# Kernel tuning notes

Measured on AMD Instinct MI355X. Metric: run time of the kernel, lower is better.

The kernel has to match this reference:

```python
import jax, jax.numpy as jnp
import numpy as np

N, G, H = 500_000, 25_000, 256


def setup_inputs() -> dict:
    key = jax.random.key(0)
    ks = jax.random.split(key, 8)
    node = jax.random.normal(ks[0], (N, H), dtype=jnp.float32)
    super_node = jax.random.normal(ks[1], (G, H), dtype=jnp.float32)
    segment_ids = jnp.sort(jax.random.randint(ks[2], (N,), 0, G, dtype=jnp.int32))
    s = 0.05
    return {
        "node": node,
        "super_node": super_node,
        "segment_ids": segment_ids,
        "w_align": jax.random.normal(ks[3], (2 * H, 1), jnp.float32) * s,
        "b_align": jnp.zeros((1,), jnp.float32),
        "w_attend": jax.random.normal(ks[4], (H, H), jnp.float32) * s,
        "b_attend": jnp.zeros((H,), jnp.float32),
        "w_ih": jax.random.normal(ks[5], (H, 3 * H), jnp.float32) * s,
        "w_hh": jax.random.normal(ks[6], (H, 3 * H), jnp.float32) * s,
        "b_ih": jnp.zeros((3 * H,), jnp.float32),
        "b_hh": jnp.zeros((3 * H,), jnp.float32),
    }


def reference(node, super_node, segment_ids, w_align, b_align, w_attend,
              b_attend, w_ih, w_hh, b_ih, b_hh):
    g = super_node.shape[0]
    h = node.shape[1]
    # super_node = F.leaky_relu(super_node)
    s = jax.nn.leaky_relu(super_node)  # slope 0.01 (torch default)
    # cal_alignment(cat([node, broadcast_nodes(super)])) == node@Wn + (s@Ws)[seg]
    wn, ws = w_align[:h], w_align[h:]
    score = jax.nn.leaky_relu(node @ wn + (s @ ws)[segment_ids] + b_align)  # [N,1]
    # softmax_nodes: segment-wise stable softmax
    m = jax.ops.segment_max(score, segment_ids, num_segments=g)
    w = jnp.exp(score - m[segment_ids])
    denom = jax.ops.segment_sum(w, segment_ids, num_segments=g)
    attn = w / denom[segment_ids]  # [N,1]
    # attend (dropout=0, eval)
    hidden = node @ w_attend + b_attend  # [N,H]
    # sum_nodes weighted by attention, then ELU
    ctx = jax.nn.elu(jax.ops.segment_sum(attn * hidden, segment_ids, num_segments=g))  # [G,H]
    # GRUCell(ctx, s) per torch semantics
    gi = ctx @ w_ih + b_ih
    gh = s @ w_hh + b_hh
    ir, iz, inn = jnp.split(gi, 3, axis=-1)
    hr, hz, hn = jnp.split(gh, 3, axis=-1)
    r = jax.nn.sigmoid(ir + hr)
    z = jax.nn.sigmoid(iz + hz)
    n = jnp.tanh(inn + r * hn)
    new_h = (1.0 - z) * n + z * s
    return jax.nn.relu(new_h), attn
```

## Files before the change

### kernel.cpp

```cpp
#include <hip/hip_runtime.h>
#include <math.h>

#define N_NODES 500000
#define G_SEG   25000
#define H_DIM   256
#define SPB     4

typedef __attribute__((ext_vector_type(4))) float f32x4;
typedef __attribute__((ext_vector_type(8))) short bf16x8;

__device__ __forceinline__ float leaky(float x){ return x > 0.f ? x : 0.01f * x; }

__device__ __forceinline__ ushort f2bf(float f){
  unsigned u = __float_as_uint(f);
  u += 0x7FFFu + ((u >> 16) & 1u);
  return (ushort)(u >> 16);
}

__global__ __launch_bounds__(256) void k_starts(
    const int* __restrict__ seg, int* __restrict__ starts)
{
  int i = blockIdx.x * 256 + threadIdx.x;
  if (i >= N_NODES) return;
  int s = seg[i];
  int prev = (i == 0) ? -1 : seg[i - 1];
  for (int g = prev + 1; g <= s; g++) starts[g] = i;
  if (i == N_NODES - 1)
    for (int g = s + 1; g <= G_SEG; g++) starts[g] = N_NODES;
}

__global__ __launch_bounds__(256) void k0_prep_w(
    const float* __restrict__ w_att, ushort* __restrict__ Bp)
{
  int kk = blockIdx.x, n = threadIdx.x;
  Bp[(((kk >> 3) << 8) + n) * 8 + (kk & 7)] = f2bf(w_att[kk * H_DIM + n]);
}

__global__ __launch_bounds__(256) void k0b_prep_w6(
    const float* __restrict__ w_ih, const float* __restrict__ w_hh,
    ushort* __restrict__ Bp6)
{
  int kk = blockIdx.x;
  int c  = threadIdx.x;
  #pragma unroll
  for (int gate = 0; gate < 4; gate++) {
    float v;
    if (gate == 0)      v = (kk < 256) ? w_ih[kk * 768 + c]        : w_hh[(kk - 256) * 768 + c];
    else if (gate == 1) v = (kk < 256) ? w_ih[kk * 768 + 256 + c]  : w_hh[(kk - 256) * 768 + 256 + c];
    else if (gate == 2) v = (kk < 256) ? w_ih[kk * 768 + 512 + c]  : 0.f;
    else                v = (kk < 256) ? 0.f                       : w_hh[(kk - 256) * 768 + 512 + c];
    int n = (gate << 8) + c;
    Bp6[(((kk >> 3) << 10) + n) * 8 + (kk & 7)] = f2bf(v);
  }
}

__global__ __launch_bounds__(256) void k1_prep_super(
    const float* __restrict__ sn, const float* __restrict__ w_align,
    float* __restrict__ s_buf, float* __restrict__ sws)
{
  int g = blockIdx.x, t = threadIdx.x;
  float v = sn[g * H_DIM + t];
  float sv = leaky(v);
  s_buf[g * H_DIM + t] = sv;
  float p = sv * w_align[H_DIM + t];
  #pragma unroll
  for (int d = 1; d < 64; d <<= 1) p += __shfl_xor(p, d);
  __shared__ float red[4];
  int wid = t >> 6, lane = t & 63;
  if (lane == 0) red[wid] = p;
  __syncthreads();
  if (t == 0) sws[g] = red[0] + red[1] + red[2] + red[3];
}

__global__ __launch_bounds__(256) void kF_score_softmax_agg(
    const float* __restrict__ node, const int* __restrict__ starts,
    const float* __restrict__ w_align, const float* __restrict__ b_align,
    const float* __restrict__ sws, float* __restrict__ score,
    float* __restrict__ attn_out, float* __restrict__ agg,
    float* __restrict__ bscale)
{
  __shared__ float cpart[4][H_DIM];
  __shared__ float wm[4], wsum[4];
  __shared__ int st_s[SPB + 1];

  const int tid = threadIdx.x;
  const int g0 = blockIdx.x * SPB;
  if (tid <= SPB) st_s[tid] = starts[g0 + tid];
  __syncthreads();

  const int wv = tid >> 6, lane = tid & 63;
  const float4 wvec = ((const float4*)w_align)[lane];
  const float b0 = b_align[0];

  for (int j = 0; j < SPB; j++) {
    const int g = g0 + j;
    const int st = st_s[j], en = st_s[j + 1];
    const float swsg = sws[g];

    float m = -3.4e38f, sum = 0.f;
    f32x4 pacc = {0.f, 0.f, 0.f, 0.f};

    for (int r = st + wv; r < en; r += 4) {
      f32x4 a = ((const f32x4*)node)[(size_t)r * 64 + lane];
      float d = a[0] * wvec.x + a[1] * wvec.y + a[2] * wvec.z + a[3] * wvec.w;
      #pragma unroll
      for (int m2 = 1; m2 < 64; m2 <<= 1) d += __shfl_xor(d, m2);
      float sc = leaky(d + swsg + b0);
      if (lane == 0) score[r] = sc;
      if (sc <= m) {
        float p = __expf(sc - m);
        sum += p;
        pacc += p * a;
      } else {
        float scale = __expf(m - sc);
        sum = sum * scale + 1.f;
        pacc = pacc * scale + a;
        m = sc;
      }
    }

    if (j > 0) __syncthreads();
    ((f32x4*)&cpart[wv][0])[lane] = pacc;
    if (lane == 0) { wm[wv] = m; wsum[wv] = sum; }
    __syncthreads();

    float m0 = fmaxf(fmaxf(wm[0], wm[1]), fmaxf(wm[2], wm[3]));
    float f0 = (wm[0] > -1e38f) ? __expf(wm[0] - m0) : 0.f;
    float f1 = (wm[1] > -1e38f) ? __expf(wm[1] - m0) : 0.f;
    float f2 = (wm[2] > -1e38f) ? __expf(wm[2] - m0) : 0.f;
    float f3 = (wm[3] > -1e38f) ? __expf(wm[3] - m0) : 0.f;
    float D = wsum[0] * f0 + wsum[1] * f1 + wsum[2] * f2 + wsum[3] * f3;
    float invD = (D > 0.f) ? 1.f / D : 0.f;

    float v = cpart[0][tid] * f0 + cpart[1][tid] * f1 +
              cpart[2][tid] * f2 + cpart[3][tid] * f3;
    agg[(size_t)g * H_DIM + tid] = v * invD;
    if (tid == 0) bscale[g] = (D > 0.f) ? 1.f : 0.f;

    for (int r = st + tid; r < en; r += 256)
      attn_out[r] = __expf(score[r] - m0) * invD;
  }
}

__global__ __launch_bounds__(256, 2) void k5b_ctx(
    const float* __restrict__ agg, const ushort* __restrict__ Bp,
    const float* __restrict__ b_att, const float* __restrict__ bscale,
    float* __restrict__ ctx)
{
  __shared__ __align__(16) ushort A_lds[128 * 256];

  const int tid  = threadIdx.x;
  const int row0 = blockIdx.x * 128;

  #pragma unroll
  for (int i = 0; i < 16; i++) {
    int v = tid + i * 256;
    int r = v >> 5;
    int s = v & 31;
    int grow = row0 + r;
    f32x4 x0 = {0.f, 0.f, 0.f, 0.f}, x1 = {0.f, 0.f, 0.f, 0.f};
    if (grow < G_SEG) {
      const f32x4* p = (const f32x4*)(agg + (size_t)grow * H_DIM) + s * 2;
      x0 = p[0]; x1 = p[1];
    }
    bf16x8 t;
    t[0] = (short)f2bf(x0[0]); t[1] = (short)f2bf(x0[1]);
    t[2] = (short)f2bf(x0[2]); t[3] = (short)f2bf(x0[3]);
    t[4] = (short)f2bf(x1[0]); t[5] = (short)f2bf(x1[1]);
    t[6] = (short)f2bf(x1[2]); t[7] = (short)f2bf(x1[3]);
    *(bf16x8*)&A_lds[r * 256 + ((s ^ (r & 7)) * 8)] = t;
  }
  __syncthreads();

  const int wv  = tid >> 6;
  const int l   = tid & 63;
  const int l15 = l & 15, lq = l >> 4, l7 = l & 7;
  const int colbase = wv * 64 + l15;

  f32x4 acc[8][4];
  #pragma unroll
  for (int mf = 0; mf < 8; mf++)
    #pragma unroll
    for (int nf = 0; nf < 4; nf++)
      acc[mf][nf] = (f32x4){0.f, 0.f, 0.f, 0.f};

  for (int ks = 0; ks < 8; ks++) {
    int c = ks * 4 + lq;
    bf16x8 b[4];
    #pragma unroll
    for (int nf = 0; nf < 4; nf++)
      b[nf] = *(const bf16x8*)&Bp[(((c << 8) + colbase + nf * 16)) * 8];
    bf16x8 a[8];
    #pragma unroll
    for (int mf = 0; mf < 8; mf++)
      a[mf] = *(const bf16x8*)&A_lds[(mf * 16 + l15) * 256 + ((c ^ l7) * 8)];
    #pragma unroll
    for (int mf = 0; mf < 8; mf++)
      #pragma unroll
      for (int nf = 0; nf < 4; nf++)
        acc[mf][nf] = __builtin_amdgcn_mfma_f32_16x16x32_bf16(
            a[mf], b[nf], acc[mf][nf], 0, 0, 0);
  }

  float bias[4];
  #pragma unroll
  for (int nf = 0; nf < 4; nf++) bias[nf] = b_att[colbase + nf * 16];

  #pragma unroll
  for (int mf = 0; mf < 8; mf++) {
    #pragma unroll
    for (int r = 0; r < 4; r++) {
      int grow = row0 + mf * 16 + lq * 4 + r;
      if (grow < G_SEG) {
        float bsc = bscale[grow];
        #pragma unroll
        for (int nf = 0; nf < 4; nf++)
          ctx[(size_t)grow * H_DIM + colbase + nf * 16] =
              acc[mf][nf][r] + bias[nf] * bsc;
      }
    }
  }
}

__global__ __launch_bounds__(256, 2) void k6_mfma(
    const float* __restrict__ ctxbuf, const float* __restrict__ s_buf,
    const ushort* __restrict__ Bp6,
    const float* __restrict__ b_ih, const float* __restrict__ b_hh,
    float* __restrict__ out0)
{
  __shared__ __align__(16) ushort A_lds[32 * 512];

  const int tid  = threadIdx.x;
  const int row0 = blockIdx.x * 32;

  #pragma unroll
  for (int i = 0; i < 8; i++) {
    int v = tid + i * 256;
    int r = v >> 6;
    int s = v & 63;
    int g = row0 + r;
    f32x4 x0 = {0.f, 0.f, 0.f, 0.f}, x1 = {0.f, 0.f, 0.f, 0.f};
    if (g < G_SEG) {
      const f32x4* p = (s < 32)
          ? (const f32x4*)(ctxbuf + (size_t)g * H_DIM) + s * 2
          : (const f32x4*)(s_buf + (size_t)g * H_DIM) + (s - 32) * 2;
      x0 = p[0]; x1 = p[1];
      if (s < 32) {
        #pragma unroll
        for (int e = 0; e < 4; e++) {
          x0[e] = x0[e] > 0.f ? x0[e] : (__expf(x0[e]) - 1.f);
          x1[e] = x1[e] > 0.f ? x1[e] : (__expf(x1[e]) - 1.f);
        }
      }
    }
    bf16x8 t;
    t[0] = (short)f2bf(x0[0]); t[1] = (short)f2bf(x0[1]);
    t[2] = (short)f2bf(x0[2]); t[3] = (short)f2bf(x0[3]);
    t[4] = (short)f2bf(x1[0]); t[5] = (short)f2bf(x1[1]);
    t[6] = (short)f2bf(x1[2]); t[7] = (short)f2bf(x1[3]);
    *(bf16x8*)&A_lds[r * 512 + ((s ^ (r & 7)) * 8)] = t;
  }
  __syncthreads();

  const int wv  = tid >> 6;
  const int l   = tid & 63;
  const int l15 = l & 15, lq = l >> 4, l7 = l & 7;

  f32x4 acc[4][2][4];
  #pragma unroll
  for (int gt = 0; gt < 4; gt++)
    #pragma unroll
    for (int mf = 0; mf < 2; mf++)
      #pragma unroll
      for (int nf = 0; nf < 4; nf++)
        acc[gt][mf][nf] = (f32x4){0.f, 0.f, 0.f, 0.f};

  for (int ks = 0; ks < 16; ks++) {
    int c = ks * 4 + lq;
    bf16x8 a[2];
    #pragma unroll
    for (int mf = 0; mf < 2; mf++)
      a[mf] = *(const bf16x8*)&A_lds[(mf * 16 + l15) * 512 + ((c ^ l7) * 8)];
    #pragma unroll
    for (int gt = 0; gt < 4; gt++) {
      if (gt == 2 && ks >= 8) continue;
      if (gt == 3 && ks < 8) continue;
      #pragma unroll
      for (int nf = 0; nf < 4; nf++) {
        int n = (gt << 8) + (wv << 6) + nf * 16 + l15;
        bf16x8 b = *(const bf16x8*)&Bp6[(((c << 10) + n)) * 8];
        acc[gt][0][nf] = __builtin_amdgcn_mfma_f32_16x16x32_bf16(
            a[0], b, acc[gt][0][nf], 0, 0, 0);
        acc[gt][1][nf] = __builtin_amdgcn_mfma_f32_16x16x32_bf16(
            a[1], b, acc[gt][1][nf], 0, 0, 0);
      }
    }
  }

  #pragma unroll
  for (int nf = 0; nf < 4; nf++) {
    int cc = (wv << 6) + nf * 16 + l15;
    float bir = b_ih[cc] + b_hh[cc];
    float biz = b_ih[256 + cc] + b_hh[256 + cc];
    float bin_ = b_ih[512 + cc];
    float bhn  = b_hh[512 + cc];
    #pragma unroll
    for (int mf = 0; mf < 2; mf++) {
      #pragma unroll
      for (int rr = 0; rr < 4; rr++) {
        int grow = row0 + mf * 16 + lq * 4 + rr;
        if (grow < G_SEG) {
          float v0 = acc[0][mf][nf][rr];
          float v1 = acc[1][mf][nf][rr];
          float v2 = acc[2][mf][nf][rr];
          float v3 = acc[3][mf][nf][rr];
          float r_ = 1.f / (1.f + __expf(-(v0 + bir)));
          float z_ = 1.f / (1.f + __expf(-(v1 + biz)));
          float n_ = tanhf(v2 + bin_ + r_ * (v3 + bhn));
          float sv = s_buf[(size_t)grow * H_DIM + cc];
          float nh = (1.f - z_) * n_ + z_ * sv;
          out0[(size_t)grow * H_DIM + cc] = nh > 0.f ? nh : 0.f;
        }
      }
    }
  }
}

extern "C" void kernel_launch(void* const* d_in, const int* in_sizes, int n_in,
                              void* d_out, int out_size, void* d_ws, size_t ws_size,
                              hipStream_t stream)
{
  (void)in_sizes; (void)n_in; (void)out_size; (void)ws_size;
  const float* node       = (const float*)d_in[0];
  const float* super_node = (const float*)d_in[1];
  const int*   seg        = (const int*)d_in[2];
  const float* w_align    = (const float*)d_in[3];
  const float* b_align    = (const float*)d_in[4];
  const float* w_att      = (const float*)d_in[5];
  const float* b_att      = (const float*)d_in[6];
  const float* w_ih       = (const float*)d_in[7];
  const float* w_hh       = (const float*)d_in[8];
  const float* b_ih       = (const float*)d_in[9];
  const float* b_hh       = (const float*)d_in[10];

  float* out0     = (float*)d_out;
  float* attn_out = (float*)d_out + (size_t)G_SEG * H_DIM;

  float* ws     = (float*)d_ws;
  float* s_buf  = ws;
  float* score  = ws + 6400000;
  float* sws    = ws + 6900000;
  float* ctx    = ws + 6925000;
  float* agg    = ws + 13325000;
  ushort* Bp    = (ushort*)(ws + 19725000);
  ushort* Bp6   = (ushort*)(ws + 19760000);
  float* bscale = ws + 20025000;
  int*   starts = (int*)(ws + 20050000);

  k_starts<<<(N_NODES + 255) / 256, 256, 0, stream>>>(seg, starts);
  k0_prep_w<<<H_DIM, H_DIM, 0, stream>>>(w_att, Bp);
  k0b_prep_w6<<<512, 256, 0, stream>>>(w_ih, w_hh, Bp6);
  k1_prep_super<<<G_SEG, 256, 0, stream>>>(super_node, w_align, s_buf, sws);
  kF_score_softmax_agg<<<G_SEG / SPB, 256, 0, stream>>>(
      node, starts, w_align, b_align, sws, score, attn_out, agg, bscale);
  k5b_ctx<<<(G_SEG + 127) / 128, 256, 0, stream>>>(agg, Bp, b_att, bscale, ctx);
  k6_mfma<<<(G_SEG + 31) / 32, 256, 0, stream>>>(ctx, s_buf, Bp6, b_ih, b_hh, out0);
}
```

Baseline: 289.1 us.

## Fuse ctx GEMM into GRU kernel, unroll softmax-agg loop, merge weight-pack kernels

Merges the attend GEMM and the GRU GEMM into one kernel, so each 32-row block computes ctx with ELU and writes it as bf16 straight into shared memory instead of a global ctx buffer. This removes one kernel launch and a full G×H fp32 round trip. The node streaming loop in the score/softmax/aggregate kernel is unrolled by four rows per wave, with batched shuffles and one online-softmax rescale per batch, to give more loads in flight. The two weight-packing kernels are also merged into one launch. The fused kernel reloads the attend weights for each 32-row block instead of each 128-row block, and uses more LDS.

```diff
diff --git a/kernel.cpp b/kernel.cpp
--- a/kernel.cpp
+++ b/kernel.cpp
@@ -29,28 +29,27 @@
     for (int g = s + 1; g <= G_SEG; g++) starts[g] = N_NODES;
 }
 
-__global__ __launch_bounds__(256) void k0_prep_w(
-    const float* __restrict__ w_att, ushort* __restrict__ Bp)
-{
-  int kk = blockIdx.x, n = threadIdx.x;
-  Bp[(((kk >> 3) << 8) + n) * 8 + (kk & 7)] = f2bf(w_att[kk * H_DIM + n]);
-}
-
-__global__ __launch_bounds__(256) void k0b_prep_w6(
-    const float* __restrict__ w_ih, const float* __restrict__ w_hh,
+__global__ __launch_bounds__(256) void kPack(
+    const float* __restrict__ w_att, const float* __restrict__ w_ih,
+    const float* __restrict__ w_hh, ushort* __restrict__ Bp,
     ushort* __restrict__ Bp6)
 {
-  int kk = blockIdx.x;
-  int c  = threadIdx.x;
-  #pragma unroll
-  for (int gate = 0; gate < 4; gate++) {
-    float v;
-    if (gate == 0)      v = (kk < 256) ? w_ih[kk * 768 + c]        : w_hh[(kk - 256) * 768 + c];
-    else if (gate == 1) v = (kk < 256) ? w_ih[kk * 768 + 256 + c]  : w_hh[(kk - 256) * 768 + 256 + c];
-    else if (gate == 2) v = (kk < 256) ? w_ih[kk * 768 + 512 + c]  : 0.f;
-    else                v = (kk < 256) ? 0.f                       : w_hh[(kk - 256) * 768 + 512 + c];
-    int n = (gate << 8) + c;
-    Bp6[(((kk >> 3) << 10) + n) * 8 + (kk & 7)] = f2bf(v);
+  int b = blockIdx.x, c = threadIdx.x;
+  if (b < 256) {
+    int kk = b;
+    Bp[(((kk >> 3) << 8) + c) * 8 + (kk & 7)] = f2bf(w_att[kk * H_DIM + c]);
+  } else {
+    int kk = b - 256;
+    #pragma unroll
+    for (int gate = 0; gate < 4; gate++) {
+      float v;
+      if (gate == 0)      v = (kk < 256) ? w_ih[kk * 768 + c]        : w_hh[(kk - 256) * 768 + c];
+      else if (gate == 1) v = (kk < 256) ? w_ih[kk * 768 + 256 + c]  : w_hh[(kk - 256) * 768 + 256 + c];
+      else if (gate == 2) v = (kk < 256) ? w_ih[kk * 768 + 512 + c]  : 0.f;
+      else                v = (kk < 256) ? 0.f                       : w_hh[(kk - 256) * 768 + 512 + c];
+      int n = (gate << 8) + c;
+      Bp6[(((kk >> 3) << 10) + n) * 8 + (kk & 7)] = f2bf(v);
+    }
   }
 }
 
@@ -100,11 +99,47 @@
     float m = -3.4e38f, sum = 0.f;
     f32x4 pacc = {0.f, 0.f, 0.f, 0.f};
 
-    for (int r = st + wv; r < en; r += 4) {
+    int r = st + wv;
+    for (; r + 12 < en; r += 16) {
+      f32x4 a0 = ((const f32x4*)node)[(size_t)(r     ) * 64 + lane];
+      f32x4 a1 = ((const f32x4*)node)[(size_t)(r +  4) * 64 + lane];
+      f32x4 a2 = ((const f32x4*)node)[(size_t)(r +  8) * 64 + lane];
+      f32x4 a3 = ((const f32x4*)node)[(size_t)(r + 12) * 64 + lane];
+      float d0 = a0[0]*wvec.x + a0[1]*wvec.y + a0[2]*wvec.z + a0[3]*wvec.w;
+      float d1 = a1[0]*wvec.x + a1[1]*wvec.y + a1[2]*wvec.z + a1[3]*wvec.w;
+      float d2 = a2[0]*wvec.x + a2[1]*wvec.y + a2[2]*wvec.z + a2[3]*wvec.w;
+      float d3 = a3[0]*wvec.x + a3[1]*wvec.y + a3[2]*wvec.z + a3[3]*wvec.w;
+      #pragma unroll
+      for (int s2 = 1; s2 < 64; s2 <<= 1) {
+        d0 += __shfl_xor(d0, s2);
+        d1 += __shfl_xor(d1, s2);
+        d2 += __shfl_xor(d2, s2);
+        d3 += __shfl_xor(d3, s2);
+      }
+      float sc0 = leaky(d0 + swsg + b0);
+      float sc1 = leaky(d1 + swsg + b0);
+      float sc2 = leaky(d2 + swsg + b0);
+      float sc3 = leaky(d3 + swsg + b0);
+      if (lane == 0) {
+        score[r] = sc0; score[r + 4] = sc1;
+        score[r + 8] = sc2; score[r + 12] = sc3;
+      }
+      float bm = fmaxf(fmaxf(sc0, sc1), fmaxf(sc2, sc3));
+      if (bm > m) {
+        float scale = __expf(m - bm);
+        sum *= scale; pacc *= scale; m = bm;
+      }
+      float p0 = __expf(sc0 - m), p1 = __expf(sc1 - m);
+      float p2 = __expf(sc2 - m), p3 = __expf(sc3 - m);
+      sum += (p0 + p1) + (p2 + p3);
+      pacc += p0 * a0 + p1 * a1;
+      pacc += p2 * a2 + p3 * a3;
+    }
+    for (; r < en; r += 4) {
       f32x4 a = ((const f32x4*)node)[(size_t)r * 64 + lane];
-      float d = a[0] * wvec.x + a[1] * wvec.y + a[2] * wvec.z + a[3] * wvec.w;
-      #pragma unroll
-      for (int m2 = 1; m2 < 64; m2 <<= 1) d += __shfl_xor(d, m2);
+      float d = a[0]*wvec.x + a[1]*wvec.y + a[2]*wvec.z + a[3]*wvec.w;
+      #pragma unroll
+      for (int s2 = 1; s2 < 64; s2 <<= 1) d += __shfl_xor(d, s2);
       float sc = leaky(d + swsg + b0);
       if (lane == 0) score[r] = sc;
       if (sc <= m) {
@@ -137,38 +172,51 @@
     agg[(size_t)g * H_DIM + tid] = v * invD;
     if (tid == 0) bscale[g] = (D > 0.f) ? 1.f : 0.f;
 
-    for (int r = st + tid; r < en; r += 256)
-      attn_out[r] = __expf(score[r] - m0) * invD;
-  }
-}
-
-__global__ __launch_bounds__(256, 2) void k5b_ctx(
-    const float* __restrict__ agg, const ushort* __restrict__ Bp,
+    for (int rr = st + tid; rr < en; rr += 256)
+      attn_out[rr] = __expf(score[rr] - m0) * invD;
+  }
+}
+
+__global__ __launch_bounds__(256, 2) void k56_fused(
+    const float* __restrict__ agg, const float* __restrict__ s_buf,
+    const ushort* __restrict__ Bp, const ushort* __restrict__ Bp6,
     const float* __restrict__ b_att, const float* __restrict__ bscale,
-    float* __restrict__ ctx)
-{
-  __shared__ __align__(16) ushort A_lds[128 * 256];
+    const float* __restrict__ b_ih, const float* __restrict__ b_hh,
+    float* __restrict__ out0)
+{
+  __shared__ __align__(16) ushort Aagg[32 * 256];
+  __shared__ __align__(16) ushort A2[32 * 512];
 
   const int tid  = threadIdx.x;
-  const int row0 = blockIdx.x * 128;
+  const int row0 = blockIdx.x * 32;
 
   #pragma unroll
-  for (int i = 0; i < 16; i++) {
+  for (int i = 0; i < 4; i++) {
     int v = tid + i * 256;
     int r = v >> 5;
     int s = v & 31;
-    int grow = row0 + r;
-    f32x4 x0 = {0.f, 0.f, 0.f, 0.f}, x1 = {0.f, 0.f, 0.f, 0.f};
-    if (grow < G_SEG) {
-      const f32x4* p = (const f32x4*)(agg + (size_t)grow * H_DIM) + s * 2;
-      x0 = p[0]; x1 = p[1];
+    int g = row0 + r;
+    f32x4 x0 = {0.f,0.f,0.f,0.f}, x1 = {0.f,0.f,0.f,0.f};
+    f32x4 y0 = {0.f,0.f,0.f,0.f}, y1 = {0.f,0.f,0.f,0.f};
+    if (g < G_SEG) {
+      const f32x4* pa = (const f32x4*)(agg + (size_t)g * H_DIM) + s * 2;
+      x0 = pa[0]; x1 = pa[1];
+      const f32x4* ps = (const f32x4*)(s_buf + (size_t)g * H_DIM) + s * 2;
+      y0 = ps[0]; y1 = ps[1];
     }
     bf16x8 t;
-    t[0] = (short)f2bf(x0[0]); t[1] = (short)f2bf(x0[1]);
-    t[2] = (short)f2bf(x0[2]); t[3] = (short)f2bf(x0[3]);
-    t[4] = (short)f2bf(x1[0]); t[5] = (short)f2bf(x1[1]);
-    t[6] = (short)f2bf(x1[2]); t[7] = (short)f2bf(x1[3]);
-    *(bf16x8*)&A_lds[r * 256 + ((s ^ (r & 7)) * 8)] = t;
+    t[0]=(short)f2bf(x0[0]); t[1]=(short)f2bf(x0[1]);
+    t[2]=(short)f2bf(x0[2]); t[3]=(short)f2bf(x0[3]);
+    t[4]=(short)f2bf(x1[0]); t[5]=(short)f2bf(x1[1]);
+    t[6]=(short)f2bf(x1[2]); t[7]=(short)f2bf(x1[3]);
+    *(bf16x8*)&Aagg[r * 256 + ((s ^ (r & 7)) * 8)] = t;
+    bf16x8 u;
+    u[0]=(short)f2bf(y0[0]); u[1]=(short)f2bf(y0[1]);
+    u[2]=(short)f2bf(y0[2]); u[3]=(short)f2bf(y0[3]);
+    u[4]=(short)f2bf(y1[0]); u[5]=(short)f2bf(y1[1]);
+    u[6]=(short)f2bf(y1[2]); u[7]=(short)f2bf(y1[3]);
+    int s2 = s + 32;
+    *(bf16x8*)&A2[r * 512 + ((s2 ^ (r & 7)) * 8)] = u;
   }
   __syncthreads();
 
@@ -177,94 +225,52 @@
   const int l15 = l & 15, lq = l >> 4, l7 = l & 7;
   const int colbase = wv * 64 + l15;
 
-  f32x4 acc[8][4];
-  #pragma unroll
-  for (int mf = 0; mf < 8; mf++)
-    #pragma unroll
-    for (int nf = 0; nf < 4; nf++)
-      acc[mf][nf] = (f32x4){0.f, 0.f, 0.f, 0.f};
-
-  for (int ks = 0; ks < 8; ks++) {
-    int c = ks * 4 + lq;
-    bf16x8 b[4];
-    #pragma unroll
-    for (int nf = 0; nf < 4; nf++)
-      b[nf] = *(const bf16x8*)&Bp[(((c << 8) + colbase + nf * 16)) * 8];
-    bf16x8 a[8];
-    #pragma unroll
-    for (int mf = 0; mf < 8; mf++)
-      a[mf] = *(const bf16x8*)&A_lds[(mf * 16 + l15) * 256 + ((c ^ l7) * 8)];
-    #pragma unroll
-    for (int mf = 0; mf < 8; mf++)
+  {
+    f32x4 acc1[2][4];
+    #pragma unroll
+    for (int mf = 0; mf < 2; mf++)
       #pragma unroll
       for (int nf = 0; nf < 4; nf++)
-        acc[mf][nf] = __builtin_amdgcn_mfma_f32_16x16x32_bf16(
-            a[mf], b[nf], acc[mf][nf], 0, 0, 0);
-  }
-
-  float bias[4];
-  #pragma unroll
-  for (int nf = 0; nf < 4; nf++) bias[nf] = b_att[colbase + nf * 16];
-
-  #pragma unroll
-  for (int mf = 0; mf < 8; mf++) {
-    #pragma unroll
-    for (int r = 0; r < 4; r++) {
-      int grow = row0 + mf * 16 + lq * 4 + r;
-      if (grow < G_SEG) {
-        float bsc = bscale[grow];
+        acc1[mf][nf] = (f32x4){0.f,0.f,0.f,0.f};
+
+    for (int ks = 0; ks < 8; ks++) {
+      int c = ks * 4 + lq;
+      bf16x8 b[4];
+      #pragma unroll
+      for (int nf = 0; nf < 4; nf++)
+        b[nf] = *(const bf16x8*)&Bp[(((c << 8) + colbase + nf * 16)) * 8];
+      bf16x8 a[2];
+      #pragma unroll
+      for (int mf = 0; mf < 2; mf++)
+        a[mf] = *(const bf16x8*)&Aagg[(mf * 16 + l15) * 256 + ((c ^ l7) * 8)];
+      #pragma unroll
+      for (int mf = 0; mf < 2; mf++)
         #pragma unroll
         for (int nf = 0; nf < 4; nf++)
-          ctx[(size_t)grow * H_DIM + colbase + nf * 16] =
-              acc[mf][nf][r] + bias[nf] * bsc;
-      }
-    }
-  }
-}
-
-__global__ __launch_bounds__(256, 2) void k6_mfma(
-    const float* __restrict__ ctxbuf, const float* __restrict__ s_buf,
-    const ushort* __restrict__ Bp6,
-    const float* __restrict__ b_ih, const float* __restrict__ b_hh,
-    float* __restrict__ out0)
-{
-  __shared__ __align__(16) ushort A_lds[32 * 512];
-
-  const int tid  = threadIdx.x;
-  const int row0 = blockIdx.x * 32;
-
-  #pragma unroll
-  for (int i = 0; i < 8; i++) {
-    int v = tid + i * 256;
-    int r = v >> 6;
-    int s = v & 63;
-    int g = row0 + r;
-    f32x4 x0 = {0.f, 0.f, 0.f, 0.f}, x1 = {0.f, 0.f, 0.f, 0.f};
-    if (g < G_SEG) {
-      const f32x4* p = (s < 32)
-          ? (const f32x4*)(ctxbuf + (size_t)g * H_DIM) + s * 2
-          : (const f32x4*)(s_buf + (size_t)g * H_DIM) + (s - 32) * 2;
-      x0 = p[0]; x1 = p[1];
-      if (s < 32) {
+          acc1[mf][nf] = __builtin_amdgcn_mfma_f32_16x16x32_bf16(
+              a[mf], b[nf], acc1[mf][nf], 0, 0, 0);
+    }
+
+    #pragma unroll
+    for (int nf = 0; nf < 4; nf++) {
+      int k = colbase + nf * 16;
+      float bias = b_att[k];
+      #pragma unroll
+      for (int mf = 0; mf < 2; mf++) {
         #pragma unroll
-        for (int e = 0; e < 4; e++) {
-          x0[e] = x0[e] > 0.f ? x0[e] : (__expf(x0[e]) - 1.f);
-          x1[e] = x1[e] > 0.f ? x1[e] : (__expf(x1[e]) - 1.f);
+        for (int rr = 0; rr < 4; rr++) {
+          int r = mf * 16 + lq * 4 + rr;
+          int grow = row0 + r;
+          float bsc = (grow < G_SEG) ? bscale[grow] : 0.f;
+          float val = acc1[mf][nf][rr] + bias * bsc;
+          val = val > 0.f ? val : (__expf(val) - 1.f);
+          int slot = (k >> 3) ^ (r & 7);
+          A2[r * 512 + slot * 8 + (k & 7)] = f2bf(val);
         }
       }
     }
-    bf16x8 t;
-    t[0] = (short)f2bf(x0[0]); t[1] = (short)f2bf(x0[1]);
-    t[2] = (short)f2bf(x0[2]); t[3] = (short)f2bf(x0[3]);
-    t[4] = (short)f2bf(x1[0]); t[5] = (short)f2bf(x1[1]);
-    t[6] = (short)f2bf(x1[2]); t[7] = (short)f2bf(x1[3]);
-    *(bf16x8*)&A_lds[r * 512 + ((s ^ (r & 7)) * 8)] = t;
   }
   __syncthreads();
-
-  const int wv  = tid >> 6;
-  const int l   = tid & 63;
-  const int l15 = l & 15, lq = l >> 4, l7 = l & 7;
 
   f32x4 acc[4][2][4];
   #pragma unroll
@@ -273,14 +279,14 @@
     for (int mf = 0; mf < 2; mf++)
       #pragma unroll
       for (int nf = 0; nf < 4; nf++)
-        acc[gt][mf][nf] = (f32x4){0.f, 0.f, 0.f, 0.f};
+        acc[gt][mf][nf] = (f32x4){0.f,0.f,0.f,0.f};
 
   for (int ks = 0; ks < 16; ks++) {
     int c = ks * 4 + lq;
     bf16x8 a[2];
     #pragma unroll
     for (int mf = 0; mf < 2; mf++)
-      a[mf] = *(const bf16x8*)&A_lds[(mf * 16 + l15) * 512 + ((c ^ l7) * 8)];
+      a[mf] = *(const bf16x8*)&A2[(mf * 16 + l15) * 512 + ((c ^ l7) * 8)];
     #pragma unroll
     for (int gt = 0; gt < 4; gt++) {
       if (gt == 2 && ks >= 8) continue;
@@ -350,19 +356,17 @@
   float* s_buf  = ws;
   float* score  = ws + 6400000;
   float* sws    = ws + 6900000;
-  float* ctx    = ws + 6925000;
-  float* agg    = ws + 13325000;
-  ushort* Bp    = (ushort*)(ws + 19725000);
-  ushort* Bp6   = (ushort*)(ws + 19760000);
-  float* bscale = ws + 20025000;
-  int*   starts = (int*)(ws + 20050000);
+  float* agg    = ws + 6925000;
+  ushort* Bp    = (ushort*)(ws + 13325000);
+  ushort* Bp6   = (ushort*)(ws + 13360000);
+  float* bscale = ws + 13625000;
+  int*   starts = (int*)(ws + 13650000);
 
   k_starts<<<(N_NODES + 255) / 256, 256, 0, stream>>>(seg, starts);
-  k0_prep_w<<<H_DIM, H_DIM, 0, stream>>>(w_att, Bp);
-  k0b_prep_w6<<<512, 256, 0, stream>>>(w_ih, w_hh, Bp6);
+  kPack<<<768, 256, 0, stream>>>(w_att, w_ih, w_hh, Bp, Bp6);
   k1_prep_super<<<G_SEG, 256, 0, stream>>>(super_node, w_align, s_buf, sws);
   kF_score_softmax_agg<<<G_SEG / SPB, 256, 0, stream>>>(
       node, starts, w_align, b_align, sws, score, attn_out, agg, bscale);
-  k5b_ctx<<<(G_SEG + 127) / 128, 256, 0, stream>>>(agg, Bp, b_att, bscale, ctx);
-  k6_mfma<<<(G_SEG + 31) / 32, 256, 0, stream>>>(ctx, s_buf, Bp6, b_ih, b_hh, out0);
-}
+  k56_fused<<<(G_SEG + 31) / 32, 256, 0, stream>>>(
+      agg, s_buf, Bp, Bp6, b_att, bscale, b_ih, b_hh, out0);
+}
```

Measured after the change: 327.7 us. 13.4% more time.
